# Performance work log

Hardware: AMD Instinct MI355X
Metric: run time of the kernel (lower is better)

## Reference

```python
import jax, jax.numpy as jnp
import numpy as np

B, T, D, H = 4, 2048, 1024, 16
DK = D // H  # 64


def setup_inputs() -> dict:
    key = jax.random.key(0)
    ks = jax.random.split(key, 8)
    std = 1.0 / np.sqrt(2.0 * D)  # initialize_weights: normal(0, 1/sqrt(2*d_model*(i_layer+1))), i_layer=0
    inp = {
        "q": jax.random.normal(ks[0], (B, T, D), jnp.float32),
        "k": jax.random.normal(ks[1], (B, T, D), jnp.float32),
        "v": jax.random.normal(ks[2], (B, T, D), jnp.float32),
        "Wq": jax.random.normal(ks[3], (D, D), jnp.float32) * std,
        "Wk": jax.random.normal(ks[4], (D, D), jnp.float32) * std,
        "Wv": jax.random.normal(ks[5], (D, D), jnp.float32) * std,
        "Wo": jax.random.normal(ks[6], (D, D), jnp.float32) * std,
        "bq": jnp.zeros((D,), jnp.float32),
        "bk": jnp.zeros((D,), jnp.float32),
        "bv": jnp.zeros((D,), jnp.float32),
        "bo": jnp.zeros((D,), jnp.float32),
    }
    return inp


def _split_heads(x):
    # (B,T,D) -> (B,H,T,DK), same as x.view(B,T,H,DK).transpose(1,2)
    b, t, _ = x.shape
    return x.reshape(b, t, H, DK).transpose(0, 2, 1, 3)


def reference(q, k, v, Wq, Wk, Wv, Wo, bq, bk, bv, bo):
    # Linear projections (torch Linear: x @ W.T + b)
    qh = _split_heads(q @ Wq.T + bq)  # (B,H,T,DK)
    kh = _split_heads(k @ Wk.T + bk)
    vh = _split_heads(v @ Wv.T + bv)

    # scaled dot-product similarities: (B,H,Tq,Tk)
    scores = jnp.einsum("bhqd,bhkd->bhqk", qh, kh) / jnp.sqrt(jnp.float32(DK))

    # causal mask: tril(ones)==0 positions filled with -inf
    tq, tk = scores.shape[-2], scores.shape[-1]
    causal = jnp.tril(jnp.ones((tq, tk), dtype=bool))
    scores = jnp.where(causal, scores, jnp.float32(-jnp.inf))

    attn = jax.nn.softmax(scores, axis=-1)  # (B,H,Tq,Tk)
    ctx = jnp.einsum("bhqk,bhkd->bhqd", attn, vh)  # (B,H,Tq,DK)

    # merge heads: (B,H,T,DK) -> (B,T,D), then output projection
    merged = ctx.transpose(0, 2, 1, 3).reshape(q.shape[0], tq, D)
    return merged @ Wo.T + bo
```

## Files before the change

kernel.cpp:

```cpp
#include <hip/hip_runtime.h>
#include <hip/hip_bf16.h>
#include <stdint.h>

#define B_ 4
#define T_ 2048
#define D_ 1024
#define H_ 16
#define DK_ 64
#define M_ (B_*T_)

typedef __attribute__((ext_vector_type(8))) short bf16x8;
typedef __attribute__((ext_vector_type(4))) short bf16x4;
typedef __attribute__((ext_vector_type(4))) float f32x4;
typedef __hip_bfloat16 bf16;

__device__ __forceinline__ void gld_lds16(const bf16* g, bf16* l) {
  __builtin_amdgcn_global_load_lds((const __attribute__((address_space(1))) void*)g,
                                   (__attribute__((address_space(3))) void*)l,
                                   16, 0, 0);
}

__device__ __forceinline__ short bfbits(float f) {
  union { bf16 h; short s; } u; u.h = __float2bfloat16(f); return u.s;
}

__global__ __launch_bounds__(256) void cvt_all(
    const float* __restrict__ q, const float* __restrict__ k, const float* __restrict__ v,
    const float* __restrict__ wq, const float* __restrict__ wk,
    const float* __restrict__ wv, const float* __restrict__ wo,
    bf16* __restrict__ qb, bf16* __restrict__ kb, bf16* __restrict__ vb,
    bf16* __restrict__ wqb, bf16* __restrict__ wkb,
    bf16* __restrict__ wvb, bf16* __restrict__ wob) {
  int gid = blockIdx.x * 256 + threadIdx.x;
  const float* src; bf16* dst; int off;
  if (gid < 6291456) {
    int s = gid >> 21; off = gid & 2097151;
    src = (s == 0) ? q : (s == 1) ? k : v;
    dst = (s == 0) ? qb : (s == 1) ? kb : vb;
  } else {
    int g2 = gid - 6291456;
    int s = g2 >> 18; off = g2 & 262143;
    src = (s == 0) ? wq : (s == 1) ? wk : (s == 2) ? wv : wo;
    dst = (s == 0) ? wqb : (s == 1) ? wkb : (s == 2) ? wvb : wob;
  }
  float4 val = reinterpret_cast<const float4*>(src)[off];
  union { ushort4 u; bf16 h[4]; } o;
  o.h[0] = __float2bfloat16(val.x);
  o.h[1] = __float2bfloat16(val.y);
  o.h[2] = __float2bfloat16(val.z);
  o.h[3] = __float2bfloat16(val.w);
  reinterpret_cast<ushort4*>(dst)[off] = o.u;
}

__global__ __launch_bounds__(512) void proj_qkv(
    const bf16* __restrict__ qb, const bf16* __restrict__ kb, const bf16* __restrict__ vb,
    const bf16* __restrict__ Wqb, const bf16* __restrict__ Wkb, const bf16* __restrict__ Wvb,
    const float* __restrict__ bq, const float* __restrict__ bk, const float* __restrict__ bv,
    bf16* __restrict__ Qh, bf16* __restrict__ Kh, bf16* __restrict__ Vt) {
  constexpr int K = 1024;
  constexpr int BK = 64;
  __shared__ __align__(16) bf16 As[256 * BK];
  __shared__ __align__(16) bf16 Bs[128 * BK];

  const int z = blockIdx.z;
  const bool vt = (z == 2);
  const bf16* A  = (z == 0) ? qb : (z == 1) ? kb : Wvb;
  const bf16* Bm = (z == 0) ? Wqb : (z == 1) ? Wkb : vb;
  const float* bias = (z == 0) ? bq : (z == 1) ? bk : bv;
  bf16* out = (z == 0) ? Qh : (z == 1) ? Kh : Vt;
  const float scale = (z == 0) ? 0.125f * 1.4426950408889634f : 1.0f;

  int bm, bn;
  if (vt) { int flat = blockIdx.x + 32 * blockIdx.y; bm = flat >> 6; bn = flat & 63; }
  else    { bm = blockIdx.x; bn = blockIdx.y; }

  const int tid = threadIdx.x;
  const int w = tid >> 6, l = tid & 63;
  const int wm = w >> 1, wn = w & 1;
  const int lr = l & 15, lk = l >> 4;

  f32x4 acc[4][4] = {};

  for (int k0 = 0; k0 < K; k0 += BK) {
#pragma unroll
    for (int i = 0; i < 4; ++i) {
      int p = i * 512 + tid;
      int row = p >> 3;
      int so = (p & 7) ^ (row & 7);
      gld_lds16(A + (size_t)(bm * 256 + row) * K + k0 + so * 8, &As[p * 8]);
    }
#pragma unroll
    for (int i = 0; i < 2; ++i) {
      int p = i * 512 + tid;
      int row = p >> 3;
      int so = (p & 7) ^ (row & 7);
      gld_lds16(Bm + (size_t)(bn * 128 + row) * K + k0 + so * 8, &Bs[p * 8]);
    }
    __syncthreads();

#pragma unroll
    for (int kk = 0; kk < 2; ++kk) {
      bf16x8 af[4], bfr[4];
#pragma unroll
      for (int m = 0; m < 4; ++m) {
        int row = wm * 64 + m * 16 + lr;
        int slot = (kk * 4 + lk) ^ (row & 7);
        af[m] = *reinterpret_cast<const bf16x8*>(&As[row * BK + slot * 8]);
      }
#pragma unroll
      for (int n = 0; n < 4; ++n) {
        int row = wn * 64 + n * 16 + lr;
        int slot = (kk * 4 + lk) ^ (row & 7);
        bfr[n] = *reinterpret_cast<const bf16x8*>(&Bs[row * BK + slot * 8]);
      }
#pragma unroll
      for (int m = 0; m < 4; ++m)
#pragma unroll
        for (int n = 0; n < 4; ++n)
          acc[m][n] = __builtin_amdgcn_mfma_f32_16x16x32_bf16(af[m], bfr[n], acc[m][n], 0, 0, 0);
    }
    __syncthreads();
  }

  const int crow0 = bm * 256 + wm * 64;
  const int ccol0 = bn * 128 + wn * 64;
#pragma unroll
  for (int m = 0; m < 4; ++m) {
#pragma unroll
    for (int n = 0; n < 4; ++n) {
#pragma unroll
      for (int r = 0; r < 4; ++r) {
        const int row = crow0 + m * 16 + lk * 4 + r;
        const int col = ccol0 + n * 16 + lr;
        if (!vt) {
          float vv = (acc[m][n][r] + bias[col]) * scale;
          size_t idx = (((size_t)(row >> 11) * H_ + (col >> 6)) * T_ + (row & (T_ - 1))) * DK_ + (col & (DK_ - 1));
          out[idx] = __float2bfloat16(vv);
        } else {
          float vv = acc[m][n][r] + bias[row];
          size_t idx = (size_t)(col >> 11) * ((size_t)H_ * DK_ * T_) + (size_t)row * T_ + (col & (T_ - 1));
          out[idx] = __float2bfloat16(vv);
        }
      }
    }
  }
}

__global__ __launch_bounds__(512) void gemm_out(const bf16* __restrict__ A,
                                                const bf16* __restrict__ Bm,
                                                const float* __restrict__ bias,
                                                float* __restrict__ Cout) {
  constexpr int K = 1024;
  constexpr int BK = 64;
  __shared__ __align__(16) bf16 As[256 * BK];
  __shared__ __align__(16) bf16 Bs[128 * BK];

  const int bm = blockIdx.x;
  const int bn = blockIdx.y;
  const int tid = threadIdx.x;
  const int w = tid >> 6, l = tid & 63;
  const int wm = w >> 1, wn = w & 1;
  const int lr = l & 15, lk = l >> 4;

  f32x4 acc[4][4] = {};

  for (int k0 = 0; k0 < K; k0 += BK) {
#pragma unroll
    for (int i = 0; i < 4; ++i) {
      int p = i * 512 + tid;
      int row = p >> 3;
      int so = (p & 7) ^ (row & 7);
      gld_lds16(A + (size_t)(bm * 256 + row) * K + k0 + so * 8, &As[p * 8]);
    }
#pragma unroll
    for (int i = 0; i < 2; ++i) {
      int p = i * 512 + tid;
      int row = p >> 3;
      int so = (p & 7) ^ (row & 7);
      gld_lds16(Bm + (size_t)(bn * 128 + row) * K + k0 + so * 8, &Bs[p * 8]);
    }
    __syncthreads();

#pragma unroll
    for (int kk = 0; kk < 2; ++kk) {
      bf16x8 af[4], bfr[4];
#pragma unroll
      for (int m = 0; m < 4; ++m) {
        int row = wm * 64 + m * 16 + lr;
        int slot = (kk * 4 + lk) ^ (row & 7);
        af[m] = *reinterpret_cast<const bf16x8*>(&As[row * BK + slot * 8]);
      }
#pragma unroll
      for (int n = 0; n < 4; ++n) {
        int row = wn * 64 + n * 16 + lr;
        int slot = (kk * 4 + lk) ^ (row & 7);
        bfr[n] = *reinterpret_cast<const bf16x8*>(&Bs[row * BK + slot * 8]);
      }
#pragma unroll
      for (int m = 0; m < 4; ++m)
#pragma unroll
        for (int n = 0; n < 4; ++n)
          acc[m][n] = __builtin_amdgcn_mfma_f32_16x16x32_bf16(af[m], bfr[n], acc[m][n], 0, 0, 0);
    }
    __syncthreads();
  }

  const int crow0 = bm * 256 + wm * 64;
  const int ccol0 = bn * 128 + wn * 64;
#pragma unroll
  for (int m = 0; m < 4; ++m) {
#pragma unroll
    for (int n = 0; n < 4; ++n) {
#pragma unroll
      for (int r = 0; r < 4; ++r) {
        const int row = crow0 + m * 16 + lk * 4 + r;
        const int col = ccol0 + n * 16 + lr;
        Cout[(size_t)row * D_ + col] = acc[m][n][r] + bias[col];
      }
    }
  }
}

__global__ __launch_bounds__(256, 4) void attn_fwd(const bf16* __restrict__ Qh,
                                                   const bf16* __restrict__ Kh,
                                                   const bf16* __restrict__ Vt,
                                                   bf16* __restrict__ ctx) {
  __shared__ __align__(16) bf16 Kbuf[2][64 * 64];
  __shared__ __align__(16) bf16 Vbuf[2][64 * 64];
  __shared__ __align__(16) char Ps[4][16 * 128];

  const int tid = threadIdx.x, w = tid >> 6, l = tid & 63;
  const int lr = l & 15, lk = l >> 4;
  const int bid = blockIdx.x;
  const int xcd = bid & 7, local = bid >> 3;
  const int hsub = local >> 4;
  const int pp = local & 15;
  char* Pw = &Ps[w][0];

  const int head = xcd * 8 + hsub;
  const bf16* Qb = Qh + (size_t)head * T_ * DK_;
  const bf16* Kb = Kh + (size_t)head * T_ * DK_;
  const bf16* Vb = Vt + (size_t)head * DK_ * T_;
  const int bb = head >> 4, hh = head & 15;

#pragma unroll 1
  for (int ti = 0; ti < 2; ++ti) {
    const int t = ti ? (31 - pp) : pp;
    const int r0 = t * 64;
    const int ntiles = t + 1;
    const int qrow = r0 + w * 16 + lr;

    const bf16* qp = Qb + (size_t)qrow * DK_ + lk * 8;
    bf16x8 qf0 = *reinterpret_cast<const bf16x8*>(qp);
    bf16x8 qf1 = *reinterpret_cast<const bf16x8*>(qp + 32);

    f32x4 oacc[4] = {};
    float srow = 0.f;

#pragma unroll
    for (int i = 0; i < 2; ++i) {
      int p = i * 256 + tid;
      int row = p >> 3;
      int so = (p & 7) ^ (row & 7);
      gld_lds16(Kb + (size_t)row * DK_ + so * 8, &Kbuf[0][p * 8]);
      gld_lds16(Vb + (size_t)row * T_ + so * 8, &Vbuf[0][p * 8]);
    }
    __syncthreads();

    int buf = 0;
#pragma unroll 1
    for (int j = 0; j < ntiles; ++j) {
      if (j + 1 < ntiles) {
        const int k0n = (j + 1) * 64;
#pragma unroll
        for (int i = 0; i < 2; ++i) {
          int p = i * 256 + tid;
          int row = p >> 3;
          int so = (p & 7) ^ (row & 7);
          gld_lds16(Kb + (size_t)(k0n + row) * DK_ + so * 8, &Kbuf[buf ^ 1][p * 8]);
          gld_lds16(Vb + (size_t)row * T_ + k0n + so * 8, &Vbuf[buf ^ 1][p * 8]);
        }
      }

      f32x4 sacc[4] = {};
      __builtin_amdgcn_s_setprio(1);
#pragma unroll
      for (int n = 0; n < 4; ++n) {
        int row = n * 16 + lr;
        int s0 = lk ^ (row & 7);
        int s1 = (4 + lk) ^ (row & 7);
        bf16x8 kf0 = *reinterpret_cast<const bf16x8*>(&Kbuf[buf][row * 64 + s0 * 8]);
        bf16x8 kf1 = *reinterpret_cast<const bf16x8*>(&Kbuf[buf][row * 64 + s1 * 8]);
        sacc[n] = __builtin_amdgcn_mfma_f32_16x16x32_bf16(kf0, qf0, sacc[n], 0, 0, 0);
        sacc[n] = __builtin_amdgcn_mfma_f32_16x16x32_bf16(kf1, qf1, sacc[n], 0, 0, 0);
      }
      __builtin_amdgcn_s_setprio(0);

      if (j == ntiles - 1) {
#pragma unroll
        for (int n = 0; n < 4; ++n)
#pragma unroll
          for (int r = 0; r < 4; ++r)
            if (j * 64 + n * 16 + lk * 4 + r > qrow) sacc[n][r] = -1e30f;
      }

      float ts = 0.f;
#pragma unroll
      for (int n = 0; n < 4; ++n) {
        float p0 = __builtin_exp2f(sacc[n][0]);
        float p1 = __builtin_exp2f(sacc[n][1]);
        float p2 = __builtin_exp2f(sacc[n][2]);
        float p3 = __builtin_exp2f(sacc[n][3]);
        ts += (p0 + p1) + (p2 + p3);
        bf16x4 pk;
        pk[0] = bfbits(p0); pk[1] = bfbits(p1); pk[2] = bfbits(p2); pk[3] = bfbits(p3);
        int swz = (n * 2 + (lk >> 1)) ^ (lr & 7);
        *reinterpret_cast<bf16x4*>(Pw + lr * 128 + swz * 16 + (lk & 1) * 8) = pk;
      }
      ts += __shfl_xor(ts, 16, 64);
      ts += __shfl_xor(ts, 32, 64);
      srow += ts;

      bf16x8 pa0 = *reinterpret_cast<const bf16x8*>(Pw + lr * 128 + ((lk ^ (lr & 7)) << 4));
      bf16x8 pa1 = *reinterpret_cast<const bf16x8*>(Pw + lr * 128 + (((4 + lk) ^ (lr & 7)) << 4));

      __builtin_amdgcn_s_setprio(1);
#pragma unroll
      for (int n = 0; n < 4; ++n) {
        int row = n * 16 + lr;
        int s0 = lk ^ (row & 7);
        int s1 = (4 + lk) ^ (row & 7);
        bf16x8 vf0 = *reinterpret_cast<const bf16x8*>(&Vbuf[buf][row * 64 + s0 * 8]);
        bf16x8 vf1 = *reinterpret_cast<const bf16x8*>(&Vbuf[buf][row * 64 + s1 * 8]);
        oacc[n] = __builtin_amdgcn_mfma_f32_16x16x32_bf16(vf0, pa0, oacc[n], 0, 0, 0);
        oacc[n] = __builtin_amdgcn_mfma_f32_16x16x32_bf16(vf1, pa1, oacc[n], 0, 0, 0);
      }
      __builtin_amdgcn_s_setprio(0);

      __syncthreads();
      buf ^= 1;
    }

    const float inv = 1.0f / srow;
#pragma unroll
    for (int n = 0; n < 4; ++n) {
      bf16x4 pk;
#pragma unroll
      for (int r = 0; r < 4; ++r) pk[r] = bfbits(oacc[n][r] * inv);
      *reinterpret_cast<bf16x4*>(&ctx[((size_t)(bb * T_ + qrow)) * D_ + hh * DK_ + n * 16 + lk * 4]) = pk;
    }
    __syncthreads();
  }
}

extern "C" void kernel_launch(void* const* d_in, const int* in_sizes, int n_in,
                              void* d_out, int out_size, void* d_ws, size_t ws_size,
                              hipStream_t stream) {
  const float* q  = (const float*)d_in[0];
  const float* k  = (const float*)d_in[1];
  const float* v  = (const float*)d_in[2];
  const float* Wq = (const float*)d_in[3];
  const float* Wk = (const float*)d_in[4];
  const float* Wv = (const float*)d_in[5];
  const float* Wo = (const float*)d_in[6];
  const float* bq = (const float*)d_in[7];
  const float* bk = (const float*)d_in[8];
  const float* bv = (const float*)d_in[9];
  const float* bo = (const float*)d_in[10];

  constexpr size_t E_IN = (size_t)M_ * D_;
  constexpr size_t E_W  = (size_t)D_ * D_;
  char* ws = (char*)d_ws;
  size_t off = 0;
  bf16* qb  = (bf16*)(ws + off); off += E_IN * 2;
  bf16* kb  = (bf16*)(ws + off); off += E_IN * 2;
  bf16* vb  = (bf16*)(ws + off); off += E_IN * 2;
  bf16* Wqb = (bf16*)(ws + off); off += E_W * 2;
  bf16* Wkb = (bf16*)(ws + off); off += E_W * 2;
  bf16* Wvb = (bf16*)(ws + off); off += E_W * 2;
  bf16* Wob = (bf16*)(ws + off); off += E_W * 2;
  bf16* Qh  = (bf16*)(ws + off); off += E_IN * 2;
  bf16* Kh  = (bf16*)(ws + off); off += E_IN * 2;
  bf16* Vtw = (bf16*)(ws + off); off += E_IN * 2;
  bf16* ctx = (bf16*)(ws + off); off += E_IN * 2;

  cvt_all<<<dim3(28672), dim3(256), 0, stream>>>(q, k, v, Wq, Wk, Wv, Wo,
                                                 qb, kb, vb, Wqb, Wkb, Wvb, Wob);

  proj_qkv<<<dim3(32, 8, 3), dim3(512), 0, stream>>>(qb, kb, vb, Wqb, Wkb, Wvb,
                                                     bq, bk, bv, Qh, Kh, Vtw);

  attn_fwd<<<dim3(1024), dim3(256), 0, stream>>>(Qh, Kh, Vtw, ctx);

  gemm_out<<<dim3(32, 8), dim3(512), 0, stream>>>(ctx, Wob, bo, (float*)d_out);
}
```

Baseline: 195.6 us.

## Fuse fp32-to-bf16 conversion of activations into the QKV projection loads

The separate conversion pass over q, k and v is removed. The projection GEMM now reads fp32 activations directly, converts them to bf16 in registers and writes them into the swizzled LDS tiles, while weights are still pre-converted. This avoids writing and rereading three bf16 activation copies. In exchange, the activation tile loads become synchronous register-staged loads instead of async global-to-LDS copies. Because each activation tile is reloaded by every column block, this also raises global read traffic in fp32.

Measured after the change: 220.3 us. +12.7%, slower.

```diff
diff --git a/kernel.cpp b/kernel.cpp
--- a/kernel.cpp
+++ b/kernel.cpp
@@ -24,25 +24,15 @@
   union { bf16 h; short s; } u; u.h = __float2bfloat16(f); return u.s;
 }
 
-__global__ __launch_bounds__(256) void cvt_all(
-    const float* __restrict__ q, const float* __restrict__ k, const float* __restrict__ v,
+__global__ __launch_bounds__(256) void cvt_w(
     const float* __restrict__ wq, const float* __restrict__ wk,
     const float* __restrict__ wv, const float* __restrict__ wo,
-    bf16* __restrict__ qb, bf16* __restrict__ kb, bf16* __restrict__ vb,
     bf16* __restrict__ wqb, bf16* __restrict__ wkb,
     bf16* __restrict__ wvb, bf16* __restrict__ wob) {
   int gid = blockIdx.x * 256 + threadIdx.x;
-  const float* src; bf16* dst; int off;
-  if (gid < 6291456) {
-    int s = gid >> 21; off = gid & 2097151;
-    src = (s == 0) ? q : (s == 1) ? k : v;
-    dst = (s == 0) ? qb : (s == 1) ? kb : vb;
-  } else {
-    int g2 = gid - 6291456;
-    int s = g2 >> 18; off = g2 & 262143;
-    src = (s == 0) ? wq : (s == 1) ? wk : (s == 2) ? wv : wo;
-    dst = (s == 0) ? wqb : (s == 1) ? wkb : (s == 2) ? wvb : wob;
-  }
+  int s = gid >> 18, off = gid & 262143;
+  const float* src = (s == 0) ? wq : (s == 1) ? wk : (s == 2) ? wv : wo;
+  bf16* dst = (s == 0) ? wqb : (s == 1) ? wkb : (s == 2) ? wvb : wob;
   float4 val = reinterpret_cast<const float4*>(src)[off];
   union { ushort4 u; bf16 h[4]; } o;
   o.h[0] = __float2bfloat16(val.x);
@@ -53,7 +43,7 @@
 }
 
 __global__ __launch_bounds__(512) void proj_qkv(
-    const bf16* __restrict__ qb, const bf16* __restrict__ kb, const bf16* __restrict__ vb,
+    const float* __restrict__ qf, const float* __restrict__ kf, const float* __restrict__ vf,
     const bf16* __restrict__ Wqb, const bf16* __restrict__ Wkb, const bf16* __restrict__ Wvb,
     const float* __restrict__ bq, const float* __restrict__ bk, const float* __restrict__ bv,
     bf16* __restrict__ Qh, bf16* __restrict__ Kh, bf16* __restrict__ Vt) {
@@ -64,8 +54,10 @@
 
   const int z = blockIdx.z;
   const bool vt = (z == 2);
-  const bf16* A  = (z == 0) ? qb : (z == 1) ? kb : Wvb;
-  const bf16* Bm = (z == 0) ? Wqb : (z == 1) ? Wkb : vb;
+  const float* Afp = (z == 0) ? qf : kf;
+  const bf16*  Abf = Wvb;
+  const float* Bfp = vf;
+  const bf16*  Bbf = (z == 0) ? Wqb : Wkb;
   const float* bias = (z == 0) ? bq : (z == 1) ? bk : bv;
   bf16* out = (z == 0) ? Qh : (z == 1) ? Kh : Vt;
   const float scale = (z == 0) ? 0.125f * 1.4426950408889634f : 1.0f;
@@ -82,19 +74,42 @@
   f32x4 acc[4][4] = {};
 
   for (int k0 = 0; k0 < K; k0 += BK) {
-#pragma unroll
-    for (int i = 0; i < 4; ++i) {
-      int p = i * 512 + tid;
-      int row = p >> 3;
-      int so = (p & 7) ^ (row & 7);
-      gld_lds16(A + (size_t)(bm * 256 + row) * K + k0 + so * 8, &As[p * 8]);
-    }
-#pragma unroll
-    for (int i = 0; i < 2; ++i) {
-      int p = i * 512 + tid;
-      int row = p >> 3;
-      int so = (p & 7) ^ (row & 7);
-      gld_lds16(Bm + (size_t)(bn * 128 + row) * K + k0 + so * 8, &Bs[p * 8]);
+    if (!vt) {
+#pragma unroll
+      for (int i = 0; i < 8; ++i) {
+        int qi = i * 512 + tid;
+        int row = qi >> 4, c4 = qi & 15;
+        float4 u = *reinterpret_cast<const float4*>(Afp + (size_t)(bm * 256 + row) * K + k0 + c4 * 4);
+        bf16x4 pk;
+        pk[0] = bfbits(u.x); pk[1] = bfbits(u.y); pk[2] = bfbits(u.z); pk[3] = bfbits(u.w);
+        int s16 = (c4 >> 1) ^ (row & 7);
+        *reinterpret_cast<bf16x4*>((char*)As + row * 128 + s16 * 16 + (c4 & 1) * 8) = pk;
+      }
+#pragma unroll
+      for (int i = 0; i < 2; ++i) {
+        int p = i * 512 + tid;
+        int row = p >> 3;
+        int so = (p & 7) ^ (row & 7);
+        gld_lds16(Bbf + (size_t)(bn * 128 + row) * K + k0 + so * 8, &Bs[p * 8]);
+      }
+    } else {
+#pragma unroll
+      for (int i = 0; i < 4; ++i) {
+        int p = i * 512 + tid;
+        int row = p >> 3;
+        int so = (p & 7) ^ (row & 7);
+        gld_lds16(Abf + (size_t)(bm * 256 + row) * K + k0 + so * 8, &As[p * 8]);
+      }
+#pragma unroll
+      for (int i = 0; i < 4; ++i) {
+        int qi = i * 512 + tid;
+        int row = qi >> 4, c4 = qi & 15;
+        float4 u = *reinterpret_cast<const float4*>(Bfp + (size_t)(bn * 128 + row) * K + k0 + c4 * 4);
+        bf16x4 pk;
+        pk[0] = bfbits(u.x); pk[1] = bfbits(u.y); pk[2] = bfbits(u.z); pk[3] = bfbits(u.w);
+        int s16 = (c4 >> 1) ^ (row & 7);
+        *reinterpret_cast<bf16x4*>((char*)Bs + row * 128 + s16 * 16 + (c4 & 1) * 8) = pk;
+      }
     }
     __syncthreads();
 
@@ -372,9 +387,6 @@
   constexpr size_t E_W  = (size_t)D_ * D_;
   char* ws = (char*)d_ws;
   size_t off = 0;
-  bf16* qb  = (bf16*)(ws + off); off += E_IN * 2;
-  bf16* kb  = (bf16*)(ws + off); off += E_IN * 2;
-  bf16* vb  = (bf16*)(ws + off); off += E_IN * 2;
   bf16* Wqb = (bf16*)(ws + off); off += E_W * 2;
   bf16* Wkb = (bf16*)(ws + off); off += E_W * 2;
   bf16* Wvb = (bf16*)(ws + off); off += E_W * 2;
@@ -384,10 +396,9 @@
   bf16* Vtw = (bf16*)(ws + off); off += E_IN * 2;
   bf16* ctx = (bf16*)(ws + off); off += E_IN * 2;
 
-  cvt_all<<<dim3(28672), dim3(256), 0, stream>>>(q, k, v, Wq, Wk, Wv, Wo,
-                                                 qb, kb, vb, Wqb, Wkb, Wvb, Wob);
-
-  proj_qkv<<<dim3(32, 8, 3), dim3(512), 0, stream>>>(qb, kb, vb, Wqb, Wkb, Wvb,
+  cvt_w<<<dim3(4096), dim3(256), 0, stream>>>(Wq, Wk, Wv, Wo, Wqb, Wkb, Wvb, Wob);
+
+  proj_qkv<<<dim3(32, 8, 3), dim3(512), 0, stream>>>(q, k, v, Wqb, Wkb, Wvb,
                                                      bq, bk, bv, Qh, Kh, Vtw);
 
   attn_fwd<<<dim3(1024), dim3(256), 0, stream>>>(Qh, Kh, Vtw, ctx);
```

## Enlarge attention query tile to 128 rows, two row-groups per wave

Applied to the files above, without the earlier changes.

Each attention block now handles 128 query rows, with every wave owning two 16-row groups, so each K/V tile loaded into LDS feeds twice as many MFMAs. The grid is halved to 512 blocks, and each block still pairs a short causal tile with a long one for balance. Waves skip K tiles beyond their causal diagonal but still join the barriers. The aim is more reuse of K/V loads and fewer redundant LDS fills, at the cost of more registers (launch bounds lowered to 2), lower occupancy and some idle waves on diagonal tiles.

Result: slower. 200.0 us (+2.2%).

```diff
diff --git a/kernel.cpp b/kernel.cpp
--- a/kernel.cpp
+++ b/kernel.cpp
@@ -221,23 +221,21 @@
   }
 }
 
-__global__ __launch_bounds__(256, 4) void attn_fwd(const bf16* __restrict__ Qh,
+__global__ __launch_bounds__(256, 2) void attn_fwd(const bf16* __restrict__ Qh,
                                                    const bf16* __restrict__ Kh,
                                                    const bf16* __restrict__ Vt,
                                                    bf16* __restrict__ ctx) {
   __shared__ __align__(16) bf16 Kbuf[2][64 * 64];
   __shared__ __align__(16) bf16 Vbuf[2][64 * 64];
-  __shared__ __align__(16) char Ps[4][16 * 128];
+  __shared__ __align__(16) char Ps[4][2][16 * 128];
 
   const int tid = threadIdx.x, w = tid >> 6, l = tid & 63;
   const int lr = l & 15, lk = l >> 4;
   const int bid = blockIdx.x;
   const int xcd = bid & 7, local = bid >> 3;
-  const int hsub = local >> 4;
-  const int pp = local & 15;
-  char* Pw = &Ps[w][0];
-
-  const int head = xcd * 8 + hsub;
+  const int head = xcd * 8 + (local >> 3);
+  const int pp = local & 7;
+
   const bf16* Qb = Qh + (size_t)head * T_ * DK_;
   const bf16* Kb = Kh + (size_t)head * T_ * DK_;
   const bf16* Vb = Vt + (size_t)head * DK_ * T_;
@@ -245,17 +243,22 @@
 
 #pragma unroll 1
   for (int ti = 0; ti < 2; ++ti) {
-    const int t = ti ? (31 - pp) : pp;
-    const int r0 = t * 64;
-    const int ntiles = t + 1;
-    const int qrow = r0 + w * 16 + lr;
-
-    const bf16* qp = Qb + (size_t)qrow * DK_ + lk * 8;
-    bf16x8 qf0 = *reinterpret_cast<const bf16x8*>(qp);
-    bf16x8 qf1 = *reinterpret_cast<const bf16x8*>(qp + 32);
-
-    f32x4 oacc[4] = {};
-    float srow = 0.f;
+    const int u = ti ? pp : (15 - pp);
+    const int base = u * 128;
+    const int ntiles = 2 * (u + 1);
+    const int jd = (base + w * 32) >> 6;
+
+    bf16x8 qf[2][2];
+#pragma unroll
+    for (int g = 0; g < 2; ++g) {
+      const int qrow = base + w * 32 + g * 16 + lr;
+      const bf16* qp = Qb + (size_t)qrow * DK_ + lk * 8;
+      qf[g][0] = *reinterpret_cast<const bf16x8*>(qp);
+      qf[g][1] = *reinterpret_cast<const bf16x8*>(qp + 32);
+    }
+
+    f32x4 oacc[2][4] = {};
+    float srow[2] = { 0.f, 0.f };
 
 #pragma unroll
     for (int i = 0; i < 2; ++i) {
@@ -282,72 +285,90 @@
         }
       }
 
-      f32x4 sacc[4] = {};
-      __builtin_amdgcn_s_setprio(1);
-#pragma unroll
-      for (int n = 0; n < 4; ++n) {
-        int row = n * 16 + lr;
-        int s0 = lk ^ (row & 7);
-        int s1 = (4 + lk) ^ (row & 7);
-        bf16x8 kf0 = *reinterpret_cast<const bf16x8*>(&Kbuf[buf][row * 64 + s0 * 8]);
-        bf16x8 kf1 = *reinterpret_cast<const bf16x8*>(&Kbuf[buf][row * 64 + s1 * 8]);
-        sacc[n] = __builtin_amdgcn_mfma_f32_16x16x32_bf16(kf0, qf0, sacc[n], 0, 0, 0);
-        sacc[n] = __builtin_amdgcn_mfma_f32_16x16x32_bf16(kf1, qf1, sacc[n], 0, 0, 0);
-      }
-      __builtin_amdgcn_s_setprio(0);
-
-      if (j == ntiles - 1) {
-#pragma unroll
-        for (int n = 0; n < 4; ++n)
-#pragma unroll
-          for (int r = 0; r < 4; ++r)
-            if (j * 64 + n * 16 + lk * 4 + r > qrow) sacc[n][r] = -1e30f;
-      }
-
-      float ts = 0.f;
-#pragma unroll
-      for (int n = 0; n < 4; ++n) {
-        float p0 = __builtin_exp2f(sacc[n][0]);
-        float p1 = __builtin_exp2f(sacc[n][1]);
-        float p2 = __builtin_exp2f(sacc[n][2]);
-        float p3 = __builtin_exp2f(sacc[n][3]);
-        ts += (p0 + p1) + (p2 + p3);
-        bf16x4 pk;
-        pk[0] = bfbits(p0); pk[1] = bfbits(p1); pk[2] = bfbits(p2); pk[3] = bfbits(p3);
-        int swz = (n * 2 + (lk >> 1)) ^ (lr & 7);
-        *reinterpret_cast<bf16x4*>(Pw + lr * 128 + swz * 16 + (lk & 1) * 8) = pk;
-      }
-      ts += __shfl_xor(ts, 16, 64);
-      ts += __shfl_xor(ts, 32, 64);
-      srow += ts;
-
-      bf16x8 pa0 = *reinterpret_cast<const bf16x8*>(Pw + lr * 128 + ((lk ^ (lr & 7)) << 4));
-      bf16x8 pa1 = *reinterpret_cast<const bf16x8*>(Pw + lr * 128 + (((4 + lk) ^ (lr & 7)) << 4));
-
-      __builtin_amdgcn_s_setprio(1);
-#pragma unroll
-      for (int n = 0; n < 4; ++n) {
-        int row = n * 16 + lr;
-        int s0 = lk ^ (row & 7);
-        int s1 = (4 + lk) ^ (row & 7);
-        bf16x8 vf0 = *reinterpret_cast<const bf16x8*>(&Vbuf[buf][row * 64 + s0 * 8]);
-        bf16x8 vf1 = *reinterpret_cast<const bf16x8*>(&Vbuf[buf][row * 64 + s1 * 8]);
-        oacc[n] = __builtin_amdgcn_mfma_f32_16x16x32_bf16(vf0, pa0, oacc[n], 0, 0, 0);
-        oacc[n] = __builtin_amdgcn_mfma_f32_16x16x32_bf16(vf1, pa1, oacc[n], 0, 0, 0);
-      }
-      __builtin_amdgcn_s_setprio(0);
+      if (j <= jd) {
+        f32x4 sacc[2][4] = {};
+        __builtin_amdgcn_s_setprio(1);
+#pragma unroll
+        for (int n = 0; n < 4; ++n) {
+          int row = n * 16 + lr;
+          int s0 = lk ^ (row & 7);
+          int s1 = (4 + lk) ^ (row & 7);
+          bf16x8 kf0 = *reinterpret_cast<const bf16x8*>(&Kbuf[buf][row * 64 + s0 * 8]);
+          bf16x8 kf1 = *reinterpret_cast<const bf16x8*>(&Kbuf[buf][row * 64 + s1 * 8]);
+          sacc[0][n] = __builtin_amdgcn_mfma_f32_16x16x32_bf16(kf0, qf[0][0], sacc[0][n], 0, 0, 0);
+          sacc[0][n] = __builtin_amdgcn_mfma_f32_16x16x32_bf16(kf1, qf[0][1], sacc[0][n], 0, 0, 0);
+          sacc[1][n] = __builtin_amdgcn_mfma_f32_16x16x32_bf16(kf0, qf[1][0], sacc[1][n], 0, 0, 0);
+          sacc[1][n] = __builtin_amdgcn_mfma_f32_16x16x32_bf16(kf1, qf[1][1], sacc[1][n], 0, 0, 0);
+        }
+        __builtin_amdgcn_s_setprio(0);
+
+        if (j == jd) {
+#pragma unroll
+          for (int g = 0; g < 2; ++g) {
+            const int qrow = base + w * 32 + g * 16 + lr;
+#pragma unroll
+            for (int n = 0; n < 4; ++n)
+#pragma unroll
+              for (int r = 0; r < 4; ++r)
+                if (j * 64 + n * 16 + lk * 4 + r > qrow) sacc[g][n][r] = -1e30f;
+          }
+        }
+
+        bf16x8 pa[2][2];
+#pragma unroll
+        for (int g = 0; g < 2; ++g) {
+          char* Pw = &Ps[w][g][0];
+          float ts = 0.f;
+#pragma unroll
+          for (int n = 0; n < 4; ++n) {
+            float p0 = __builtin_exp2f(sacc[g][n][0]);
+            float p1 = __builtin_exp2f(sacc[g][n][1]);
+            float p2 = __builtin_exp2f(sacc[g][n][2]);
+            float p3 = __builtin_exp2f(sacc[g][n][3]);
+            ts += (p0 + p1) + (p2 + p3);
+            bf16x4 pk;
+            pk[0] = bfbits(p0); pk[1] = bfbits(p1); pk[2] = bfbits(p2); pk[3] = bfbits(p3);
+            int swz = (n * 2 + (lk >> 1)) ^ (lr & 7);
+            *reinterpret_cast<bf16x4*>(Pw + lr * 128 + swz * 16 + (lk & 1) * 8) = pk;
+          }
+          ts += __shfl_xor(ts, 16, 64);
+          ts += __shfl_xor(ts, 32, 64);
+          srow[g] += ts;
+          pa[g][0] = *reinterpret_cast<const bf16x8*>(Pw + lr * 128 + ((lk ^ (lr & 7)) << 4));
+          pa[g][1] = *reinterpret_cast<const bf16x8*>(Pw + lr * 128 + (((4 + lk) ^ (lr & 7)) << 4));
+        }
+
+        __builtin_amdgcn_s_setprio(1);
+#pragma unroll
+        for (int n = 0; n < 4; ++n) {
+          int row = n * 16 + lr;
+          int s0 = lk ^ (row & 7);
+          int s1 = (4 + lk) ^ (row & 7);
+          bf16x8 vf0 = *reinterpret_cast<const bf16x8*>(&Vbuf[buf][row * 64 + s0 * 8]);
+          bf16x8 vf1 = *reinterpret_cast<const bf16x8*>(&Vbuf[buf][row * 64 + s1 * 8]);
+          oacc[0][n] = __builtin_amdgcn_mfma_f32_16x16x32_bf16(vf0, pa[0][0], oacc[0][n], 0, 0, 0);
+          oacc[0][n] = __builtin_amdgcn_mfma_f32_16x16x32_bf16(vf1, pa[0][1], oacc[0][n], 0, 0, 0);
+          oacc[1][n] = __builtin_amdgcn_mfma_f32_16x16x32_bf16(vf0, pa[1][0], oacc[1][n], 0, 0, 0);
+          oacc[1][n] = __builtin_amdgcn_mfma_f32_16x16x32_bf16(vf1, pa[1][1], oacc[1][n], 0, 0, 0);
+        }
+        __builtin_amdgcn_s_setprio(0);
+      }
 
       __syncthreads();
       buf ^= 1;
     }
 
-    const float inv = 1.0f / srow;
-#pragma unroll
-    for (int n = 0; n < 4; ++n) {
-      bf16x4 pk;
-#pragma unroll
-      for (int r = 0; r < 4; ++r) pk[r] = bfbits(oacc[n][r] * inv);
-      *reinterpret_cast<bf16x4*>(&ctx[((size_t)(bb * T_ + qrow)) * D_ + hh * DK_ + n * 16 + lk * 4]) = pk;
+#pragma unroll
+    for (int g = 0; g < 2; ++g) {
+      const float inv = 1.0f / srow[g];
+      const int qrow = base + w * 32 + g * 16 + lr;
+#pragma unroll
+      for (int n = 0; n < 4; ++n) {
+        bf16x4 pk;
+#pragma unroll
+        for (int r = 0; r < 4; ++r) pk[r] = bfbits(oacc[g][n][r] * inv);
+        *reinterpret_cast<bf16x4*>(&ctx[((size_t)(bb * T_ + qrow)) * D_ + hh * DK_ + n * 16 + lk * 4]) = pk;
+      }
     }
     __syncthreads();
   }
@@ -390,7 +411,7 @@
   proj_qkv<<<dim3(32, 8, 3), dim3(512), 0, stream>>>(qb, kb, vb, Wqb, Wkb, Wvb,
                                                      bq, bk, bv, Qh, Kh, Vtw);
 
-  attn_fwd<<<dim3(1024), dim3(256), 0, stream>>>(Qh, Kh, Vtw, ctx);
+  attn_fwd<<<dim3(512), dim3(256), 0, stream>>>(Qh, Kh, Vtw, ctx);
 
   gemm_out<<<dim3(32, 8), dim3(512), 0, stream>>>(ctx, Wob, bo, (float*)d_out);
 }
```

## Split attention into one q-tile per block with 32-key tiles

Applied to the files above, without the earlier changes.

The attention kernel now launches one block per (head, query tile), with tiles ordered longest first, instead of pairing two complementary query tiles per block. KV tiles shrink from 64 to 32 keys, which halves LDS use, and launch bounds rise so more blocks fit per CU. Each wave skips compute on 32-key tiles beyond its own diagonal, which trims masked work. In exchange there are twice as many barriers and loads per key, and load balance now depends on the scheduler rather than on the explicit pairing.

Result: no change. 191.8 us (-1.9%).

```diff
diff --git a/kernel.cpp b/kernel.cpp
--- a/kernel.cpp
+++ b/kernel.cpp
@@ -221,71 +221,70 @@
   }
 }
 
-__global__ __launch_bounds__(256, 4) void attn_fwd(const bf16* __restrict__ Qh,
+__global__ __launch_bounds__(256, 7) void attn_fwd(const bf16* __restrict__ Qh,
                                                    const bf16* __restrict__ Kh,
                                                    const bf16* __restrict__ Vt,
                                                    bf16* __restrict__ ctx) {
-  __shared__ __align__(16) bf16 Kbuf[2][64 * 64];
-  __shared__ __align__(16) bf16 Vbuf[2][64 * 64];
-  __shared__ __align__(16) char Ps[4][16 * 128];
+  __shared__ __align__(16) bf16 Kbuf[2][32 * 64];
+  __shared__ __align__(16) bf16 Vbuf[2][32 * 64];
+  __shared__ __align__(16) char Ps[4][16 * 80];
 
   const int tid = threadIdx.x, w = tid >> 6, l = tid & 63;
   const int lr = l & 15, lk = l >> 4;
   const int bid = blockIdx.x;
-  const int xcd = bid & 7, local = bid >> 3;
-  const int hsub = local >> 4;
-  const int pp = local & 15;
+  const int head = bid & 63;
+  const int t = 31 - (bid >> 6);
   char* Pw = &Ps[w][0];
 
-  const int head = xcd * 8 + hsub;
   const bf16* Qb = Qh + (size_t)head * T_ * DK_;
   const bf16* Kb = Kh + (size_t)head * T_ * DK_;
   const bf16* Vb = Vt + (size_t)head * DK_ * T_;
   const int bb = head >> 4, hh = head & 15;
 
+  const int r0 = t * 64;
+  const int nt32 = 2 * (t + 1);
+  const int qrow = r0 + w * 16 + lr;
+  const int jd = (r0 + w * 16) >> 5;
+
+  const bf16* qp = Qb + (size_t)qrow * DK_ + lk * 8;
+  bf16x8 qf0 = *reinterpret_cast<const bf16x8*>(qp);
+  bf16x8 qf1 = *reinterpret_cast<const bf16x8*>(qp + 32);
+
+  f32x4 oacc[4] = {};
+  float srow = 0.f;
+
+  {
+    int p = tid;
+    int krow = p >> 3;
+    int kso = (p & 7) ^ (krow & 7);
+    gld_lds16(Kb + (size_t)krow * DK_ + kso * 8, &Kbuf[0][p * 8]);
+    int vrow = p >> 3;
+    int u = (p & 7) ^ (vrow & 7);
+    int dk = vrow * 2 + (u >> 2);
+    gld_lds16(Vb + (size_t)dk * T_ + (u & 3) * 8, &Vbuf[0][p * 8]);
+  }
+  __syncthreads();
+
+  int buf = 0;
 #pragma unroll 1
-  for (int ti = 0; ti < 2; ++ti) {
-    const int t = ti ? (31 - pp) : pp;
-    const int r0 = t * 64;
-    const int ntiles = t + 1;
-    const int qrow = r0 + w * 16 + lr;
-
-    const bf16* qp = Qb + (size_t)qrow * DK_ + lk * 8;
-    bf16x8 qf0 = *reinterpret_cast<const bf16x8*>(qp);
-    bf16x8 qf1 = *reinterpret_cast<const bf16x8*>(qp + 32);
-
-    f32x4 oacc[4] = {};
-    float srow = 0.f;
-
-#pragma unroll
-    for (int i = 0; i < 2; ++i) {
-      int p = i * 256 + tid;
-      int row = p >> 3;
-      int so = (p & 7) ^ (row & 7);
-      gld_lds16(Kb + (size_t)row * DK_ + so * 8, &Kbuf[0][p * 8]);
-      gld_lds16(Vb + (size_t)row * T_ + so * 8, &Vbuf[0][p * 8]);
-    }
-    __syncthreads();
-
-    int buf = 0;
-#pragma unroll 1
-    for (int j = 0; j < ntiles; ++j) {
-      if (j + 1 < ntiles) {
-        const int k0n = (j + 1) * 64;
-#pragma unroll
-        for (int i = 0; i < 2; ++i) {
-          int p = i * 256 + tid;
-          int row = p >> 3;
-          int so = (p & 7) ^ (row & 7);
-          gld_lds16(Kb + (size_t)(k0n + row) * DK_ + so * 8, &Kbuf[buf ^ 1][p * 8]);
-          gld_lds16(Vb + (size_t)row * T_ + k0n + so * 8, &Vbuf[buf ^ 1][p * 8]);
-        }
-      }
-
-      f32x4 sacc[4] = {};
+  for (int j = 0; j < nt32; ++j) {
+    if (j + 1 < nt32) {
+      const int k0n = (j + 1) * 32;
+      int p = tid;
+      int krow = p >> 3;
+      int kso = (p & 7) ^ (krow & 7);
+      gld_lds16(Kb + (size_t)(k0n + krow) * DK_ + kso * 8, &Kbuf[buf ^ 1][p * 8]);
+      int vrow = p >> 3;
+      int u = (p & 7) ^ (vrow & 7);
+      int dk = vrow * 2 + (u >> 2);
+      gld_lds16(Vb + (size_t)dk * T_ + k0n + (u & 3) * 8, &Vbuf[buf ^ 1][p * 8]);
+    }
+
+    if (j <= jd) {
+      f32x4 sacc[2] = {};
       __builtin_amdgcn_s_setprio(1);
 #pragma unroll
-      for (int n = 0; n < 4; ++n) {
+      for (int n = 0; n < 2; ++n) {
         int row = n * 16 + lr;
         int s0 = lk ^ (row & 7);
         int s1 = (4 + lk) ^ (row & 7);
@@ -296,17 +295,17 @@
       }
       __builtin_amdgcn_s_setprio(0);
 
-      if (j == ntiles - 1) {
-#pragma unroll
-        for (int n = 0; n < 4; ++n)
+      if (j == jd) {
+#pragma unroll
+        for (int n = 0; n < 2; ++n)
 #pragma unroll
           for (int r = 0; r < 4; ++r)
-            if (j * 64 + n * 16 + lk * 4 + r > qrow) sacc[n][r] = -1e30f;
+            if (j * 32 + n * 16 + lk * 4 + r > qrow) sacc[n][r] = -1e30f;
       }
 
       float ts = 0.f;
 #pragma unroll
-      for (int n = 0; n < 4; ++n) {
+      for (int n = 0; n < 2; ++n) {
         float p0 = __builtin_exp2f(sacc[n][0]);
         float p1 = __builtin_exp2f(sacc[n][1]);
         float p2 = __builtin_exp2f(sacc[n][2]);
@@ -314,42 +313,37 @@
         ts += (p0 + p1) + (p2 + p3);
         bf16x4 pk;
         pk[0] = bfbits(p0); pk[1] = bfbits(p1); pk[2] = bfbits(p2); pk[3] = bfbits(p3);
-        int swz = (n * 2 + (lk >> 1)) ^ (lr & 7);
-        *reinterpret_cast<bf16x4*>(Pw + lr * 128 + swz * 16 + (lk & 1) * 8) = pk;
+        *reinterpret_cast<bf16x4*>(Pw + lr * 80 + n * 32 + lk * 8) = pk;
       }
       ts += __shfl_xor(ts, 16, 64);
       ts += __shfl_xor(ts, 32, 64);
       srow += ts;
 
-      bf16x8 pa0 = *reinterpret_cast<const bf16x8*>(Pw + lr * 128 + ((lk ^ (lr & 7)) << 4));
-      bf16x8 pa1 = *reinterpret_cast<const bf16x8*>(Pw + lr * 128 + (((4 + lk) ^ (lr & 7)) << 4));
+      bf16x8 pa = *reinterpret_cast<const bf16x8*>(Pw + lr * 80 + lk * 16);
 
       __builtin_amdgcn_s_setprio(1);
 #pragma unroll
       for (int n = 0; n < 4; ++n) {
-        int row = n * 16 + lr;
-        int s0 = lk ^ (row & 7);
-        int s1 = (4 + lk) ^ (row & 7);
-        bf16x8 vf0 = *reinterpret_cast<const bf16x8*>(&Vbuf[buf][row * 64 + s0 * 8]);
-        bf16x8 vf1 = *reinterpret_cast<const bf16x8*>(&Vbuf[buf][row * 64 + s1 * 8]);
-        oacc[n] = __builtin_amdgcn_mfma_f32_16x16x32_bf16(vf0, pa0, oacc[n], 0, 0, 0);
-        oacc[n] = __builtin_amdgcn_mfma_f32_16x16x32_bf16(vf1, pa1, oacc[n], 0, 0, 0);
+        int rowp = n * 8 + (lr >> 1);
+        int u = (lr & 1) * 4 + lk;
+        int s = u ^ (rowp & 7);
+        bf16x8 vf = *reinterpret_cast<const bf16x8*>(&Vbuf[buf][rowp * 64 + s * 8]);
+        oacc[n] = __builtin_amdgcn_mfma_f32_16x16x32_bf16(vf, pa, oacc[n], 0, 0, 0);
       }
       __builtin_amdgcn_s_setprio(0);
-
-      __syncthreads();
-      buf ^= 1;
-    }
-
-    const float inv = 1.0f / srow;
-#pragma unroll
-    for (int n = 0; n < 4; ++n) {
-      bf16x4 pk;
-#pragma unroll
-      for (int r = 0; r < 4; ++r) pk[r] = bfbits(oacc[n][r] * inv);
-      *reinterpret_cast<bf16x4*>(&ctx[((size_t)(bb * T_ + qrow)) * D_ + hh * DK_ + n * 16 + lk * 4]) = pk;
-    }
-    __syncthreads();
+    }
+
+    __syncthreads();
+    buf ^= 1;
+  }
+
+  const float inv = 1.0f / srow;
+#pragma unroll
+  for (int n = 0; n < 4; ++n) {
+    bf16x4 pk;
+#pragma unroll
+    for (int r = 0; r < 4; ++r) pk[r] = bfbits(oacc[n][r] * inv);
+    *reinterpret_cast<bf16x4*>(&ctx[((size_t)(bb * T_ + qrow)) * D_ + hh * DK_ + n * 16 + lk * 4]) = pk;
   }
 }
 
@@ -390,7 +384,7 @@
   proj_qkv<<<dim3(32, 8, 3), dim3(512), 0, stream>>>(qb, kb, vb, Wqb, Wkb, Wvb,
                                                      bq, bk, bv, Qh, Kh, Vtw);
 
-  attn_fwd<<<dim3(1024), dim3(256), 0, stream>>>(Qh, Kh, Vtw, ctx);
+  attn_fwd<<<dim3(2048), dim3(256), 0, stream>>>(Qh, Kh, Vtw, ctx);
 
   gemm_out<<<dim3(32, 8), dim3(512), 0, stream>>>(ctx, Wob, bo, (float*)d_out);
 }
```
